# Performance work log

Measured on AMD Instinct MI355X. Metric: run time of the kernel, lower is better.

## Reference

```python
import jax, jax.numpy as jnp
import numpy as np

D_MODEL = 1024
N_HEADS = 16
D_K = D_MODEL // N_HEADS
EPS = 1e-6


def setup_inputs() -> dict:
    key = jax.random.key(0)
    ks = jax.random.split(key, 9)
    s = 1.0 / np.sqrt(D_MODEL)
    x = jax.random.normal(ks[0], (4, 4096, D_MODEL), dtype=jnp.float32)
    Wq = jax.random.uniform(ks[1], (D_MODEL, D_MODEL), jnp.float32, -s, s)
    bq = jax.random.uniform(ks[2], (D_MODEL,), jnp.float32, -s, s)
    Wk = jax.random.uniform(ks[3], (D_MODEL, D_MODEL), jnp.float32, -s, s)
    bk = jax.random.uniform(ks[4], (D_MODEL,), jnp.float32, -s, s)
    Wv = jax.random.uniform(ks[5], (D_MODEL, D_MODEL), jnp.float32, -s, s)
    bv = jax.random.uniform(ks[6], (D_MODEL,), jnp.float32, -s, s)
    Wo = jax.random.uniform(ks[7], (D_MODEL, D_MODEL), jnp.float32, -s, s)
    bo = jax.random.uniform(ks[8], (D_MODEL,), jnp.float32, -s, s)
    return {"x": x, "Wq": Wq, "bq": bq, "Wk": Wk, "bk": bk,
            "Wv": Wv, "bv": bv, "Wo": Wo, "bo": bo}


def _feature_map(t):
    # elu(x) + 1
    return jax.nn.elu(t) + 1.0


def reference(x, Wq, bq, Wk, bk, Wv, bv, Wo, bo):
    b, s, _ = x.shape
    # projections, split into heads: [b, h, s, d_k]
    def heads(t):
        return t.reshape(b, s, N_HEADS, D_K).transpose(0, 2, 1, 3)
    q = _feature_map(heads(x @ Wq + bq))
    k = _feature_map(heads(x @ Wk + bk))
    v = heads(x @ Wv + bv)
    # kv accumulation: [b, h, d_k, d_k]
    kv = jnp.einsum('bhsd,bhse->bhde', k, v)
    # normalizer: q . sum_s k  -> [b, h, s, 1]
    z = jnp.einsum('bhsd,bhd->bhs', q, k.sum(axis=2))[..., None]
    out = jnp.einsum('bhsd,bhde->bhse', q, kv) / (z + EPS)
    out = out.transpose(0, 2, 1, 3).reshape(b, s, D_MODEL)
    return out @ Wo + bo
```

## Files before the change

kernel.cpp:

```cpp
#include <hip/hip_runtime.h>


typedef __bf16 bf16;
typedef float  f32x4  __attribute__((ext_vector_type(4)));
typedef short  s16x8  __attribute__((ext_vector_type(8)));
typedef bf16   bf16x4 __attribute__((ext_vector_type(4)));

#define BATCH 4
#define SEQ   4096
#define DM    1024
#define NH    16
#define DK    64
#define MROWS (BATCH*SEQ)
#define EPSV  1e-6f

__device__ __forceinline__ void async_cp16(const bf16* g, bf16* l) {
  __builtin_amdgcn_global_load_lds((const __attribute__((address_space(1))) void*)g,
                                   (__attribute__((address_space(3))) void*)l,
                                   16, 0, 0);
}

__global__ __launch_bounds__(256) void conv_x_kernel(const float* __restrict__ x,
                                                     bf16* __restrict__ xb) {
  int i = (blockIdx.x * 256 + threadIdx.x) * 4;
  float4 f = *reinterpret_cast<const float4*>(x + i);
  bf16x4 o;
  o[0] = (bf16)f.x; o[1] = (bf16)f.y; o[2] = (bf16)f.z; o[3] = (bf16)f.w;
  *reinterpret_cast<bf16x4*>(xb + i) = o;
}

__global__ __launch_bounds__(256) void conv_w_kernel(const float* __restrict__ W0,
                                                     const float* __restrict__ W1,
                                                     const float* __restrict__ W2,
                                                     const float* __restrict__ W3,
                                                     bf16* __restrict__ Wt) {
  __shared__ bf16 tt[64][72];
  const int z = blockIdx.z;
  const float* W = (z == 0) ? W0 : (z == 1) ? W1 : (z == 2) ? W2 : W3;
  const int n0 = blockIdx.x * 64, k0 = blockIdx.y * 64;
  const int tid = threadIdx.x;
#pragma unroll
  for (int i = 0; i < 4; ++i) {
    const int c = tid + i * 256;
    const int krow = c >> 4, nch = c & 15;
    float4 f = *reinterpret_cast<const float4*>(W + (size_t)(k0 + krow) * DM + n0 + nch * 4);
    tt[nch * 4 + 0][krow] = (bf16)f.x;
    tt[nch * 4 + 1][krow] = (bf16)f.y;
    tt[nch * 4 + 2][krow] = (bf16)f.z;
    tt[nch * 4 + 3][krow] = (bf16)f.w;
  }
  __syncthreads();
#pragma unroll
  for (int i = 0; i < 2; ++i) {
    const int c = tid + i * 256;
    const int nrow = c >> 3, kch = c & 7;
    *reinterpret_cast<uint4*>(Wt + (size_t)(z * DM + n0 + nrow) * DM + k0 + kch * 8) =
        *reinterpret_cast<const uint4*>(&tt[nrow][kch * 8]);
  }
}

template <int MODE>
__global__ __launch_bounds__(512, 2) void gemm_bf16(const bf16* __restrict__ A,
                                                    const bf16* __restrict__ Bt,
                                                    void* __restrict__ Cout, int ldc,
                                                    const float* __restrict__ b0,
                                                    const float* __restrict__ b1,
                                                    const float* __restrict__ b2) {
  constexpr int K  = 1024;
  constexpr int BK = 64;
  constexpr int NT = K / BK;
  __shared__ __align__(16) char smem[131072];

  const int tid  = threadIdx.x;
  const int wv   = tid >> 6, lane = tid & 63;
  const int quad = lane >> 4, l16 = lane & 15;
  const int swk  = l16 & 7;

  const int nwg = gridDim.x * gridDim.y;
  int lin = blockIdx.y * gridDim.x + blockIdx.x;
  lin = (lin & 7) * (nwg >> 3) + (lin >> 3);
  const int bm0 = (lin & 63) << 8;
  const int bn0 = (lin >> 6) << 8;

  const int wm = wv >> 2;
  const int wn = wv & 3;

  f32x4 acc[8][4] = {};
  s16x8 af[4][2];
  s16x8 bq[2][2][2];

  const int srow = wv * 8 + (lane >> 3);
  const int scol = ((lane & 7) ^ (lane >> 3)) * 8;
  const bf16* Ag = A  + (size_t)(bm0 + srow) * K + scol;
  const bf16* Bg = Bt + (size_t)(bn0 + srow) * K + scol;
  const int sbase = wv * 1024;

#define STAGE_A(t_, h_) do {                                                   \
    const bf16* g_ = Ag + (size_t)((h_) * 128) * K + (t_) * BK;                \
    char* l_ = smem + ((t_) & 1) * 32768 + (h_) * 16384 + sbase;               \
    async_cp16(g_, (bf16*)l_);                                                 \
    async_cp16(g_ + (size_t)64 * K, (bf16*)(l_ + 8192));                       \
  } while (0)
#define STAGE_B(t_, h_) do {                                                   \
    const bf16* g_ = Bg + (size_t)((h_) * 128) * K + (t_) * BK;                \
    char* l_ = smem + 65536 + ((t_) & 1) * 32768 + (h_) * 16384 + sbase;       \
    async_cp16(g_, (bf16*)l_);                                                 \
    async_cp16(g_ + (size_t)64 * K, (bf16*)(l_ + 8192));                       \
  } while (0)
#define LDA(pb_, qm_) do {                                                     \
    const char* ab_ = smem + (pb_) * 32768 +                                   \
        (size_t)(wm * 128 + (qm_) * 64 + l16) * 128;                           \
    _Pragma("unroll") for (int mi = 0; mi < 4; ++mi)                           \
      _Pragma("unroll") for (int ks = 0; ks < 2; ++ks)                         \
        af[mi][ks] = *reinterpret_cast<const s16x8*>(                          \
            ab_ + mi * 2048 + (((ks * 4 + quad) ^ swk) << 4));                 \
  } while (0)
#define LDB(pb_, qn_) do {                                                     \
    const char* bb_ = smem + 65536 + (pb_) * 32768 +                           \
        (size_t)(wn * 64 + (qn_) * 32 + l16) * 128;                            \
    _Pragma("unroll") for (int ni = 0; ni < 2; ++ni)                           \
      _Pragma("unroll") for (int ks = 0; ks < 2; ++ks)                         \
        bq[qn_][ni][ks] = *reinterpret_cast<const s16x8*>(                     \
            bb_ + ni * 2048 + (((ks * 4 + quad) ^ swk) << 4));                 \
  } while (0)
#define MFMA_Q(qm_, qn_) do {                                                  \
    _Pragma("unroll") for (int mi = 0; mi < 4; ++mi)                           \
      _Pragma("unroll") for (int ni = 0; ni < 2; ++ni)                         \
        _Pragma("unroll") for (int ks = 0; ks < 2; ++ks)                       \
          acc[(qm_) * 4 + mi][(qn_) * 2 + ni] =                                \
              __builtin_amdgcn_mfma_f32_16x16x32_bf16(                         \
                  af[mi][ks], bq[qn_][ni][ks],                                 \
                  acc[(qm_) * 4 + mi][(qn_) * 2 + ni], 0, 0, 0);               \
  } while (0)

  STAGE_B(0, 0); STAGE_A(0, 0); STAGE_B(0, 1); STAGE_A(0, 1);
  STAGE_B(1, 0); STAGE_A(1, 0);
  asm volatile("s_waitcnt vmcnt(4)");
  __builtin_amdgcn_s_barrier();
  __builtin_amdgcn_sched_barrier(0);
  LDA(0, 0); LDB(0, 0); LDB(0, 1);
  __builtin_amdgcn_sched_barrier(0);

#pragma unroll 2
  for (int t = 0; t < NT; ++t) {
    const int p = t & 1;
    if (t + 1 < NT) STAGE_B(t + 1, 1);
    asm volatile("s_waitcnt lgkmcnt(0)");
    __builtin_amdgcn_sched_barrier(0);
    __builtin_amdgcn_s_setprio(1);
    MFMA_Q(0, 0); MFMA_Q(0, 1);
    __builtin_amdgcn_s_setprio(0);
    LDA(p, 1);
    __builtin_amdgcn_sched_barrier(0);
    if (t + 1 < NT) STAGE_A(t + 1, 1);
    asm volatile("s_waitcnt lgkmcnt(0)");
    __builtin_amdgcn_sched_barrier(0);
    __builtin_amdgcn_s_setprio(1);
    MFMA_Q(1, 0); MFMA_Q(1, 1);
    __builtin_amdgcn_s_setprio(0);
    __builtin_amdgcn_s_barrier();
    __builtin_amdgcn_sched_barrier(0);
    if (t + 2 < NT) { STAGE_B(t + 2, 0); STAGE_A(t + 2, 0); }
    if (t + 1 < NT) {
      if (t + 2 < NT) asm volatile("s_waitcnt vmcnt(4)");
      else            asm volatile("s_waitcnt vmcnt(0)");
      __builtin_amdgcn_s_barrier();
      __builtin_amdgcn_sched_barrier(0);
      LDA(p ^ 1, 0); LDB(p ^ 1, 0); LDB(p ^ 1, 1);
      __builtin_amdgcn_sched_barrier(0);
    }
  }

  if (MODE == 0) {
    const int part = bn0 >> 10;
    const float* bp = (part == 0) ? b0 : (part == 1) ? b1 : b2;
    bf16* C = (bf16*)Cout;
    bf16 (*Cw)[64] = (bf16(*)[64])(smem + wv * 16384);
#pragma unroll
    for (int ni = 0; ni < 4; ++ni) {
      const int n_l = ni * 16 + l16;
      const float bias = bp[(bn0 + wn * 64 + n_l) & 1023];
#pragma unroll
      for (int mi = 0; mi < 8; ++mi)
#pragma unroll
        for (int r = 0; r < 4; ++r) {
          float v = acc[mi][ni][r] + bias;
          if (part < 2) v = (v > 0.f) ? (v + 1.f) : __expf(v);
          const int row = mi * 16 + quad * 4 + r;
          Cw[row][n_l ^ ((row & 7) << 3)] = (bf16)v;
        }
    }
#pragma unroll
    for (int i = 0; i < 16; ++i) {
      const int row = i * 8 + (lane >> 3), ch = lane & 7;
      *reinterpret_cast<uint4*>(C + (size_t)(bm0 + wm * 128 + row) * ldc +
                                bn0 + wn * 64 + ch * 8) =
          *reinterpret_cast<const uint4*>(&Cw[row][(ch ^ (row & 7)) * 8]);
    }
  } else {
    float* C = (float*)Cout;
    float (*Cwf)[64] = (float(*)[64])(smem + wv * 16384);
#pragma unroll
    for (int h = 0; h < 2; ++h) {
#pragma unroll
      for (int ni = 0; ni < 4; ++ni) {
        const int n_l = ni * 16 + l16;
        const float bias = b0[bn0 + wn * 64 + n_l];
#pragma unroll
        for (int mi = 0; mi < 4; ++mi)
#pragma unroll
          for (int r = 0; r < 4; ++r) {
            const int row = mi * 16 + quad * 4 + r;
            Cwf[row][n_l ^ ((row & 7) << 2)] = acc[h * 4 + mi][ni][r] + bias;
          }
      }
#pragma unroll
      for (int i = 0; i < 16; ++i) {
        const int row = i * 4 + (lane >> 4), ch = lane & 15;
        *reinterpret_cast<float4*>(C + (size_t)(bm0 + wm * 128 + h * 64 + row) * ldc +
                                   bn0 + wn * 64 + ch * 4) =
            *reinterpret_cast<const float4*>(&Cwf[row][(ch ^ (row & 7)) * 4]);
      }
    }
  }
#undef STAGE_A
#undef STAGE_B
#undef LDA
#undef LDB
#undef MFMA_Q
}

__global__ __launch_bounds__(256) void kv_ksum_kernel(const bf16* __restrict__ QKV,
                                                      float* __restrict__ kvT,
                                                      float* __restrict__ ksum) {
  __shared__ bf16 Ks[128][64];
  __shared__ bf16 Vs[128][64];
  const int bh = blockIdx.y;
  const int b = bh >> 4, h = bh & 15;
  const int tid = threadIdx.x;
  const int d0 = (tid >> 4) * 4, e0 = (tid & 15) * 4;
  const size_t base = (size_t)b * SEQ * 3072;
  const int colK = 1024 + h * 64, colV = 2048 + h * 64;

  float acc[4][4] = {};
  float ks4[4] = {};

  for (int cc = 0; cc < 4; ++cc) {
    const int s0 = blockIdx.x * 512 + cc * 128;
#pragma unroll
    for (int i = 0; i < 4; ++i) {
      const int c = tid + i * 256;
      const int row = c >> 3, off = (c & 7) * 8;
      const size_t roff = base + (size_t)(s0 + row) * 3072;
      *reinterpret_cast<uint4*>(&Ks[row][off]) =
          *reinterpret_cast<const uint4*>(QKV + roff + colK + off);
      *reinterpret_cast<uint4*>(&Vs[row][off]) =
          *reinterpret_cast<const uint4*>(QKV + roff + colV + off);
    }
    __syncthreads();
#pragma unroll 4
    for (int s = 0; s < 128; ++s) {
      bf16x4 kk = *reinterpret_cast<const bf16x4*>(&Ks[s][d0]);
      bf16x4 vv = *reinterpret_cast<const bf16x4*>(&Vs[s][e0]);
      float kd[4], ve[4];
#pragma unroll
      for (int j = 0; j < 4; ++j) { kd[j] = (float)kk[j]; ve[j] = (float)vv[j]; }
#pragma unroll
      for (int i = 0; i < 4; ++i) {
        ks4[i] += kd[i];
#pragma unroll
        for (int j = 0; j < 4; ++j) acc[i][j] += kd[i] * ve[j];
      }
    }
    __syncthreads();
  }
#pragma unroll
  for (int i = 0; i < 4; ++i)
#pragma unroll
    for (int j = 0; j < 4; ++j)
      atomicAdd(&kvT[(size_t)bh * 4096 + (e0 + j) * 64 + (d0 + i)], acc[i][j]);
  if ((tid & 15) == 0) {
#pragma unroll
    for (int i = 0; i < 4; ++i)
      atomicAdd(&ksum[bh * 64 + d0 + i], ks4[i]);
  }
}

__global__ __launch_bounds__(256) void attn_kernel(const bf16* __restrict__ QKV,
                                                   const float* __restrict__ kvT,
                                                   const float* __restrict__ ksum,
                                                   bf16* __restrict__ ATT) {
  __shared__ bf16 qs[128][72];
  __shared__ bf16 kvs[64][72];
  __shared__ bf16 Ps[128][72];
  __shared__ float zr[128];
  __shared__ float kss[64];
  const int bh = blockIdx.y;
  const int b = bh >> 4, h = bh & 15;
  const int s0 = blockIdx.x * 128;
  const int tid = threadIdx.x, wave = tid >> 6, lane = tid & 63;
  const int quad = lane >> 4, l16 = lane & 15;
  const size_t base = (size_t)b * SEQ * 3072;
  const int colQ = h * 64;

#pragma unroll
  for (int i = 0; i < 4; ++i) {
    const int c = tid + i * 256;
    const int row = c >> 3, off = (c & 7) * 8;
    *reinterpret_cast<uint4*>(&qs[row][off]) =
        *reinterpret_cast<const uint4*>(QKV + base + (size_t)(s0 + row) * 3072 + colQ + off);
  }
  const float* kvg = kvT + (size_t)bh * 4096;
#pragma unroll
  for (int i = 0; i < 4; ++i) {
    const int c = tid + i * 256;
    const int row = c >> 4, off = (c & 15) * 4;
    float4 f = *reinterpret_cast<const float4*>(kvg + row * 64 + off);
    bf16x4 o;
    o[0] = (bf16)f.x; o[1] = (bf16)f.y; o[2] = (bf16)f.z; o[3] = (bf16)f.w;
    *reinterpret_cast<bf16x4*>(&kvs[row][off]) = o;
  }
  if (tid < 64) kss[tid] = ksum[bh * 64 + tid];
  __syncthreads();

  if (tid < 128) {
    float z = 0.f;
#pragma unroll
    for (int d = 0; d < 64; d += 4) {
      bf16x4 q4 = *reinterpret_cast<const bf16x4*>(&qs[tid][d]);
      z += (float)q4[0] * kss[d] + (float)q4[1] * kss[d + 1] +
           (float)q4[2] * kss[d + 2] + (float)q4[3] * kss[d + 3];
    }
    zr[tid] = 1.0f / (z + EPSV);
  }
  __syncthreads();

  const int wn = wave * 32;
  f32x4 pacc[4][2] = {};
#pragma unroll
  for (int ks = 0; ks < 2; ++ks) {
    s16x8 af[4], bf2[2];
#pragma unroll
    for (int mi = 0; mi < 4; ++mi)
      af[mi] = *reinterpret_cast<const s16x8*>(&kvs[mi * 16 + l16][ks * 32 + quad * 8]);
#pragma unroll
    for (int ni = 0; ni < 2; ++ni)
      bf2[ni] = *reinterpret_cast<const s16x8*>(&qs[wn + ni * 16 + l16][ks * 32 + quad * 8]);
#pragma unroll
    for (int mi = 0; mi < 4; ++mi)
#pragma unroll
      for (int ni = 0; ni < 2; ++ni)
        pacc[mi][ni] = __builtin_amdgcn_mfma_f32_16x16x32_bf16(af[mi], bf2[ni],
                                                               pacc[mi][ni], 0, 0, 0);
  }
#pragma unroll
  for (int ni = 0; ni < 2; ++ni) {
    const int s = wn + ni * 16 + l16;
    const float zi = zr[s];
#pragma unroll
    for (int mi = 0; mi < 4; ++mi) {
      bf16x4 o;
#pragma unroll
      for (int r = 0; r < 4; ++r) o[r] = (bf16)(pacc[mi][ni][r] * zi);
      *reinterpret_cast<bf16x4*>(&Ps[s][mi * 16 + quad * 4]) = o;
    }
  }
  __syncthreads();
#pragma unroll
  for (int i = 0; i < 4; ++i) {
    const int c = tid + i * 256;
    const int row = c >> 3, ch = c & 7;
    *reinterpret_cast<uint4*>(ATT + ((size_t)b * SEQ + s0 + row) * DM + h * 64 + ch * 8) =
        *reinterpret_cast<const uint4*>(&Ps[row][ch * 8]);
  }
}

extern "C" void kernel_launch(void* const* d_in, const int* in_sizes, int n_in,
                              void* d_out, int out_size, void* d_ws, size_t ws_size,
                              hipStream_t stream) {
  const float* x  = (const float*)d_in[0];
  const float* Wq = (const float*)d_in[1];
  const float* bq = (const float*)d_in[2];
  const float* Wk = (const float*)d_in[3];
  const float* bk = (const float*)d_in[4];
  const float* Wv = (const float*)d_in[5];
  const float* bv = (const float*)d_in[6];
  const float* Wo = (const float*)d_in[7];
  const float* bo = (const float*)d_in[8];
  float* out = (float*)d_out;

  char* ws = (char*)d_ws;
  bf16*  Xb   = (bf16*)ws;   ws += (size_t)MROWS * DM * 2;
  bf16*  Wt   = (bf16*)ws;   ws += (size_t)4 * DM * DM * 2;
  bf16*  QKV  = (bf16*)ws;   ws += (size_t)MROWS * 3 * DM * 2;
  bf16*  ATT  = (bf16*)ws;   ws += (size_t)MROWS * DM * 2;
  float* kvT  = (float*)ws;  ws += (size_t)64 * 4096 * 4;
  float* ksum = (float*)ws;  ws += (size_t)64 * 64 * 4;

  (void)hipMemsetAsync(kvT, 0, (size_t)64 * 4096 * 4 + (size_t)64 * 64 * 4, stream);

  conv_x_kernel<<<MROWS * DM / 1024, 256, 0, stream>>>(x, Xb);
  conv_w_kernel<<<dim3(16, 16, 4), 256, 0, stream>>>(Wq, Wk, Wv, Wo, Wt);
  gemm_bf16<0><<<dim3(12, 64), 512, 0, stream>>>(Xb, Wt, QKV, 3 * DM, bq, bk, bv);
  kv_ksum_kernel<<<dim3(8, 64), 256, 0, stream>>>(QKV, kvT, ksum);
  attn_kernel<<<dim3(32, 64), 256, 0, stream>>>(QKV, kvT, ksum, ATT);
  gemm_bf16<1><<<dim3(4, 64), 512, 0, stream>>>(ATT, Wt + (size_t)3 * DM * DM, out, DM, bo, bo, bo);
}
```

Before: 370.9 us.

## Store K/V transposed from QKV GEMM epilogue and compute KV with MFMA

```diff
diff --git a/kernel.cpp b/kernel.cpp
--- a/kernel.cpp
+++ b/kernel.cpp
@@ -65,7 +65,9 @@
                                                     void* __restrict__ Cout, int ldc,
                                                     const float* __restrict__ b0,
                                                     const float* __restrict__ b1,
-                                                    const float* __restrict__ b2) {
+                                                    const float* __restrict__ b2,
+                                                    bf16* __restrict__ kt,
+                                                    bf16* __restrict__ vt) {
   constexpr int K  = 1024;
   constexpr int BK = 64;
   constexpr int NT = K / BK;
@@ -76,11 +78,10 @@
   const int quad = lane >> 4, l16 = lane & 15;
   const int swk  = l16 & 7;
 
-  const int nwg = gridDim.x * gridDim.y;
-  int lin = blockIdx.y * gridDim.x + blockIdx.x;
-  lin = (lin & 7) * (nwg >> 3) + (lin >> 3);
-  const int bm0 = (lin & 63) << 8;
-  const int bn0 = (lin >> 6) << 8;
+  const int w = blockIdx.y * gridDim.x + blockIdx.x;
+  const int j = w >> 3;
+  const int bm0 = (((w & 7) << 3) + (j & 7)) << 8;
+  const int bn0 = (j >> 3) << 8;
 
   const int wm = wv >> 2;
   const int wn = wv & 3;
@@ -173,29 +174,63 @@
 
   if (MODE == 0) {
     const int part = bn0 >> 10;
-    const float* bp = (part == 0) ? b0 : (part == 1) ? b1 : b2;
-    bf16* C = (bf16*)Cout;
-    bf16 (*Cw)[64] = (bf16(*)[64])(smem + wv * 16384);
-#pragma unroll
-    for (int ni = 0; ni < 4; ++ni) {
-      const int n_l = ni * 16 + l16;
-      const float bias = bp[(bn0 + wn * 64 + n_l) & 1023];
-#pragma unroll
-      for (int mi = 0; mi < 8; ++mi)
-#pragma unroll
-        for (int r = 0; r < 4; ++r) {
-          float v = acc[mi][ni][r] + bias;
-          if (part < 2) v = (v > 0.f) ? (v + 1.f) : __expf(v);
-          const int row = mi * 16 + quad * 4 + r;
-          Cw[row][n_l ^ ((row & 7) << 3)] = (bf16)v;
+    if (part == 0) {
+      bf16* C = (bf16*)Cout;
+      bf16 (*Cw)[64] = (bf16(*)[64])(smem + wv * 16384);
+#pragma unroll
+      for (int ni = 0; ni < 4; ++ni) {
+        const int n_l = ni * 16 + l16;
+        const float bias = b0[bn0 + wn * 64 + n_l];
+#pragma unroll
+        for (int mi = 0; mi < 8; ++mi)
+#pragma unroll
+          for (int r = 0; r < 4; ++r) {
+            float v = acc[mi][ni][r] + bias;
+            v = (v > 0.f) ? (v + 1.f) : __expf(v);
+            const int row = mi * 16 + quad * 4 + r;
+            Cw[row][n_l ^ ((row & 7) << 3)] = (bf16)v;
+          }
+      }
+#pragma unroll
+      for (int i = 0; i < 16; ++i) {
+        const int row = i * 8 + (lane >> 3), ch = lane & 7;
+        *reinterpret_cast<uint4*>(C + (size_t)(bm0 + wm * 128 + row) * ldc +
+                                  bn0 + wn * 64 + ch * 8) =
+            *reinterpret_cast<const uint4*>(&Cw[row][(ch ^ (row & 7)) * 8]);
+      }
+    } else {
+      bf16* T = (part == 1) ? kt : vt;
+      const float* bp = (part == 1) ? b1 : b2;
+      const int b  = bm0 >> 12;
+      const int h  = ((bn0 & 1023) >> 6) + wn;
+      const int s_loc = (bm0 & 4095) + wm * 128;
+      bf16* base = T + (size_t)(b * 16 + h) * 64 * 4096 + s_loc;
+      char* sl = smem + wv * 16384;
+#pragma unroll
+      for (int ni = 0; ni < 4; ++ni) {
+        const int d = ni * 16 + l16;
+        const float bias = bp[(bn0 + wn * 64 + d) & 1023];
+#pragma unroll
+        for (int mi = 0; mi < 8; ++mi) {
+          bf16x4 o;
+#pragma unroll
+          for (int r = 0; r < 4; ++r) {
+            float v = acc[mi][ni][r] + bias;
+            if (part == 1) v = (v > 0.f) ? (v + 1.f) : __expf(v);
+            o[r] = (bf16)v;
+          }
+          const int sb = mi * 32 + quad * 8;
+          *reinterpret_cast<uint2*>(sl + d * 256 + (sb ^ ((d & 7) << 4))) =
+              *reinterpret_cast<const uint2*>(&o);
         }
-    }
-#pragma unroll
-    for (int i = 0; i < 16; ++i) {
-      const int row = i * 8 + (lane >> 3), ch = lane & 7;
-      *reinterpret_cast<uint4*>(C + (size_t)(bm0 + wm * 128 + row) * ldc +
-                                bn0 + wn * 64 + ch * 8) =
-          *reinterpret_cast<const uint4*>(&Cw[row][(ch ^ (row & 7)) * 8]);
+      }
+#pragma unroll
+      for (int i = 0; i < 16; ++i) {
+        const int d = i * 4 + (lane >> 4), ch = l16;
+        const uint4 val = *reinterpret_cast<const uint4*>(
+            sl + d * 256 + ((ch * 16) ^ ((d & 7) << 4)));
+        *reinterpret_cast<uint4*>(base + (size_t)d * 4096 + ch * 8) = val;
+      }
     }
   } else {
     float* C = (float*)Cout;
@@ -230,63 +265,79 @@
 #undef MFMA_Q
 }
 
-__global__ __launch_bounds__(256) void kv_ksum_kernel(const bf16* __restrict__ QKV,
-                                                      float* __restrict__ kvT,
-                                                      float* __restrict__ ksum) {
-  __shared__ bf16 Ks[128][64];
-  __shared__ bf16 Vs[128][64];
+__global__ __launch_bounds__(256) void kvk_mfma_kernel(const bf16* __restrict__ KT,
+                                                       const bf16* __restrict__ VT,
+                                                       float* __restrict__ kvT,
+                                                       float* __restrict__ ksum) {
+  __shared__ bf16 Ks[64][136];
+  __shared__ bf16 Vs[64][136];
   const int bh = blockIdx.y;
-  const int b = bh >> 4, h = bh & 15;
   const int tid = threadIdx.x;
-  const int d0 = (tid >> 4) * 4, e0 = (tid & 15) * 4;
-  const size_t base = (size_t)b * SEQ * 3072;
-  const int colK = 1024 + h * 64, colV = 2048 + h * 64;
-
-  float acc[4][4] = {};
-  float ks4[4] = {};
+  const int wv = tid >> 6, lane = tid & 63;
+  const int quad = lane >> 4, l16 = lane & 15;
+  const size_t tb = (size_t)bh * 64 * 4096;
+  const int s0b = blockIdx.x * 512;
+
+  f32x4 acc[4][4] = {};
+  float ksp[4] = {};
 
   for (int cc = 0; cc < 4; ++cc) {
-    const int s0 = blockIdx.x * 512 + cc * 128;
+    const int s0 = s0b + cc * 128;
+    __syncthreads();
 #pragma unroll
     for (int i = 0; i < 4; ++i) {
       const int c = tid + i * 256;
-      const int row = c >> 3, off = (c & 7) * 8;
-      const size_t roff = base + (size_t)(s0 + row) * 3072;
-      *reinterpret_cast<uint4*>(&Ks[row][off]) =
-          *reinterpret_cast<const uint4*>(QKV + roff + colK + off);
-      *reinterpret_cast<uint4*>(&Vs[row][off]) =
-          *reinterpret_cast<const uint4*>(QKV + roff + colV + off);
+      const int row = c >> 4, ch = c & 15;
+      const size_t go = tb + (size_t)row * 4096 + s0 + ch * 8;
+      uint4 kk = *reinterpret_cast<const uint4*>(KT + go);
+      *reinterpret_cast<uint4*>(&Ks[row][ch * 8]) = kk;
+      *reinterpret_cast<uint4*>(&Vs[row][ch * 8]) =
+          *reinterpret_cast<const uint4*>(VT + go);
+      const bf16* kp = reinterpret_cast<const bf16*>(&kk);
+      float t = 0.f;
+#pragma unroll
+      for (int jj = 0; jj < 8; ++jj) t += (float)kp[jj];
+      ksp[i] += t;
     }
     __syncthreads();
-#pragma unroll 4
-    for (int s = 0; s < 128; ++s) {
-      bf16x4 kk = *reinterpret_cast<const bf16x4*>(&Ks[s][d0]);
-      bf16x4 vv = *reinterpret_cast<const bf16x4*>(&Vs[s][e0]);
-      float kd[4], ve[4];
-#pragma unroll
-      for (int j = 0; j < 4; ++j) { kd[j] = (float)kk[j]; ve[j] = (float)vv[j]; }
-#pragma unroll
-      for (int i = 0; i < 4; ++i) {
-        ks4[i] += kd[i];
-#pragma unroll
-        for (int j = 0; j < 4; ++j) acc[i][j] += kd[i] * ve[j];
-      }
-    }
-    __syncthreads();
-  }
+    const int kb = wv * 32 + quad * 8;
+    s16x8 vfr[4], kfr[4];
+#pragma unroll
+    for (int mi = 0; mi < 4; ++mi) {
+      vfr[mi] = *reinterpret_cast<const s16x8*>(&Vs[mi * 16 + l16][kb]);
+      kfr[mi] = *reinterpret_cast<const s16x8*>(&Ks[mi * 16 + l16][kb]);
+    }
+#pragma unroll
+    for (int mi = 0; mi < 4; ++mi)
+#pragma unroll
+      for (int ni = 0; ni < 4; ++ni)
+        acc[mi][ni] = __builtin_amdgcn_mfma_f32_16x16x32_bf16(vfr[mi], kfr[ni],
+                                                              acc[mi][ni], 0, 0, 0);
+  }
+#pragma unroll
+  for (int mi = 0; mi < 4; ++mi)
+#pragma unroll
+    for (int ni = 0; ni < 4; ++ni)
+#pragma unroll
+      for (int r = 0; r < 4; ++r) {
+        const int e = mi * 16 + quad * 4 + r;
+        const int d = ni * 16 + l16;
+        atomicAdd(&kvT[(size_t)bh * 4096 + e * 64 + d], acc[mi][ni][r]);
+      }
 #pragma unroll
   for (int i = 0; i < 4; ++i)
 #pragma unroll
-    for (int j = 0; j < 4; ++j)
-      atomicAdd(&kvT[(size_t)bh * 4096 + (e0 + j) * 64 + (d0 + i)], acc[i][j]);
-  if ((tid & 15) == 0) {
+    for (int o = 8; o > 0; o >>= 1)
+      ksp[i] += __shfl_down(ksp[i], o, 16);
+  if (l16 == 0) {
+    const int g = tid >> 4;
 #pragma unroll
     for (int i = 0; i < 4; ++i)
-      atomicAdd(&ksum[bh * 64 + d0 + i], ks4[i]);
-  }
-}
-
-__global__ __launch_bounds__(256) void attn_kernel(const bf16* __restrict__ QKV,
+      atomicAdd(&ksum[bh * 64 + g + 16 * i], ksp[i]);
+  }
+}
+
+__global__ __launch_bounds__(256) void attn_kernel(const bf16* __restrict__ Qb,
                                                    const float* __restrict__ kvT,
                                                    const float* __restrict__ ksum,
                                                    bf16* __restrict__ ATT) {
@@ -300,7 +351,7 @@
   const int s0 = blockIdx.x * 128;
   const int tid = threadIdx.x, wave = tid >> 6, lane = tid & 63;
   const int quad = lane >> 4, l16 = lane & 15;
-  const size_t base = (size_t)b * SEQ * 3072;
+  const size_t base = (size_t)b * SEQ * DM;
   const int colQ = h * 64;
 
 #pragma unroll
@@ -308,7 +359,7 @@
     const int c = tid + i * 256;
     const int row = c >> 3, off = (c & 7) * 8;
     *reinterpret_cast<uint4*>(&qs[row][off]) =
-        *reinterpret_cast<const uint4*>(QKV + base + (size_t)(s0 + row) * 3072 + colQ + off);
+        *reinterpret_cast<const uint4*>(Qb + base + (size_t)(s0 + row) * DM + colQ + off);
   }
   const float* kvg = kvT + (size_t)bh * 4096;
 #pragma unroll
@@ -392,7 +443,9 @@
   char* ws = (char*)d_ws;
   bf16*  Xb   = (bf16*)ws;   ws += (size_t)MROWS * DM * 2;
   bf16*  Wt   = (bf16*)ws;   ws += (size_t)4 * DM * DM * 2;
-  bf16*  QKV  = (bf16*)ws;   ws += (size_t)MROWS * 3 * DM * 2;
+  bf16*  Qb   = (bf16*)ws;   ws += (size_t)MROWS * DM * 2;
+  bf16*  KT   = (bf16*)ws;   ws += (size_t)64 * 64 * 4096 * 2;
+  bf16*  VT   = (bf16*)ws;   ws += (size_t)64 * 64 * 4096 * 2;
   bf16*  ATT  = (bf16*)ws;   ws += (size_t)MROWS * DM * 2;
   float* kvT  = (float*)ws;  ws += (size_t)64 * 4096 * 4;
   float* ksum = (float*)ws;  ws += (size_t)64 * 64 * 4;
@@ -401,8 +454,9 @@
 
   conv_x_kernel<<<MROWS * DM / 1024, 256, 0, stream>>>(x, Xb);
   conv_w_kernel<<<dim3(16, 16, 4), 256, 0, stream>>>(Wq, Wk, Wv, Wo, Wt);
-  gemm_bf16<0><<<dim3(12, 64), 512, 0, stream>>>(Xb, Wt, QKV, 3 * DM, bq, bk, bv);
-  kv_ksum_kernel<<<dim3(8, 64), 256, 0, stream>>>(QKV, kvT, ksum);
-  attn_kernel<<<dim3(32, 64), 256, 0, stream>>>(QKV, kvT, ksum, ATT);
-  gemm_bf16<1><<<dim3(4, 64), 512, 0, stream>>>(ATT, Wt + (size_t)3 * DM * DM, out, DM, bo, bo, bo);
-}
+  gemm_bf16<0><<<dim3(12, 64), 512, 0, stream>>>(Xb, Wt, Qb, DM, bq, bk, bv, KT, VT);
+  kvk_mfma_kernel<<<dim3(8, 64), 256, 0, stream>>>(KT, VT, kvT, ksum);
+  attn_kernel<<<dim3(32, 64), 256, 0, stream>>>(Qb, kvT, ksum, ATT);
+  gemm_bf16<1><<<dim3(4, 64), 512, 0, stream>>>(ATT, Wt + (size_t)3 * DM * DM, out, DM,
+                                                bo, bo, bo, nullptr, nullptr);
+}
```

Result: faster. 342.5 us (-7.7%).
